# Performance work log

Hardware: AMD Instinct MI355X
Metric: run time of the kernel (lower is better)

Reference implementation:

```python
import jax, jax.numpy as jnp
import numpy as np

N = 1_000_000
C = 128
B = 16  # number of instances (batch segments)
EPS = 1e-5


def setup_inputs() -> dict:
    key = jax.random.key(0)
    k1, k2 = jax.random.split(key)
    x = jax.random.normal(k1, (N, C), dtype=jnp.float32)
    batch_idx = jnp.sort(jax.random.randint(k2, (N,), 0, B, dtype=jnp.int32))
    weight = jnp.ones((1, C), dtype=jnp.float32)
    bias = jnp.zeros((1, C), dtype=jnp.float32)
    return {"x": x, "batch_idx": batch_idx, "weight": weight, "bias": bias}


def reference(x, batch_idx, weight, bias):
    # per-instance counts [B, 1]
    cnt = jax.ops.segment_sum(jnp.ones((x.shape[0], 1), x.dtype), batch_idx,
                              num_segments=B)
    cnt = jnp.maximum(cnt, 1.0)
    # segment mean [B, C]
    mean = jax.ops.segment_sum(x, batch_idx, num_segments=B) / cnt
    centered = x - mean[batch_idx]               # broadcast-add of -mean
    # segment mean of squared centered features -> per-instance variance [B, C]
    var = jax.ops.segment_sum(centered * centered, batch_idx, num_segments=B) / cnt
    instd = 1.0 / jnp.sqrt(var + EPS)            # [B, C]
    # broadcast-multiply, then affine
    return centered * instd[batch_idx] * weight + bias
```

## Files before the change

kernel.cpp:

```cpp
#include <hip/hip_runtime.h>

#define CC 128
#define BSEG 16
#define EPSV 1e-5f
#define ROWS_PER_BLOCK 512
#define NORM_GRID 2048

typedef float v4f __attribute__((ext_vector_type(4)));

__global__ __launch_bounds__(256) void ms_stats(const float* __restrict__ x,
                                                const int* __restrict__ bidx,
                                                int n,
                                                float* __restrict__ sum,
                                                float* __restrict__ sumsq,
                                                float* __restrict__ cnt)
{
    const int r0 = blockIdx.x * ROWS_PER_BLOCK;
    if (r0 >= n) return;
    const int rend = min(r0 + ROWS_PER_BLOCK, n);
    const int tq = threadIdx.x & 31;
    const int tr = threadIdx.x >> 5;

    const int seg_first = bidx[r0];
    const int seg_last  = bidx[rend - 1];

    v4f s = {0.f, 0.f, 0.f, 0.f};
    v4f q = {0.f, 0.f, 0.f, 0.f};

    if (seg_first == seg_last) {
        int r = r0 + tr;
        for (; r + 8 < rend; r += 16) {
            const v4f a = *reinterpret_cast<const v4f*>(x + (size_t)r * CC + tq * 4);
            const v4f b = *reinterpret_cast<const v4f*>(x + (size_t)(r + 8) * CC + tq * 4);
            s += a; q += a * a;
            s += b; q += b * b;
        }
        if (r < rend) {
            const v4f a = *reinterpret_cast<const v4f*>(x + (size_t)r * CC + tq * 4);
            s += a; q += a * a;
        }
        __shared__ float red[8][8][32];
        red[tr][0][tq] = s.x; red[tr][1][tq] = s.y; red[tr][2][tq] = s.z; red[tr][3][tq] = s.w;
        red[tr][4][tq] = q.x; red[tr][5][tq] = q.y; red[tr][6][tq] = q.z; red[tr][7][tq] = q.w;
        __syncthreads();
        const int j = threadIdx.x >> 5;
        float acc = 0.f;
        #pragma unroll
        for (int k = 0; k < 8; ++k) acc += red[k][j][tq];
        const int ch = tq * 4 + (j & 3);
        atomicAdd(((j < 4) ? sum : sumsq) + seg_first * CC + ch, acc);
        if (threadIdx.x == 0)
            atomicAdd(cnt + seg_first, (float)(rend - r0));
    } else {
        int cur = -1;
        float rows = 0.f;
        for (int r = r0 + tr; r < rend; r += 8) {
            const int seg = bidx[r];
            if (seg != cur) {
                if (cur >= 0) {
                    float* sd = sum   + cur * CC + tq * 4;
                    float* qd = sumsq + cur * CC + tq * 4;
                    atomicAdd(sd + 0, s.x); atomicAdd(sd + 1, s.y);
                    atomicAdd(sd + 2, s.z); atomicAdd(sd + 3, s.w);
                    atomicAdd(qd + 0, q.x); atomicAdd(qd + 1, q.y);
                    atomicAdd(qd + 2, q.z); atomicAdd(qd + 3, q.w);
                    if (tq == 0) atomicAdd(cnt + cur, rows);
                    s = (v4f){0.f, 0.f, 0.f, 0.f};
                    q = (v4f){0.f, 0.f, 0.f, 0.f};
                    rows = 0.f;
                }
                cur = seg;
            }
            const v4f a = *reinterpret_cast<const v4f*>(x + (size_t)r * CC + tq * 4);
            s += a; q += a * a;
            rows += 1.f;
        }
        if (cur >= 0) {
            float* sd = sum   + cur * CC + tq * 4;
            float* qd = sumsq + cur * CC + tq * 4;
            atomicAdd(sd + 0, s.x); atomicAdd(sd + 1, s.y);
            atomicAdd(sd + 2, s.z); atomicAdd(sd + 3, s.w);
            atomicAdd(qd + 0, q.x); atomicAdd(qd + 1, q.y);
            atomicAdd(qd + 2, q.z); atomicAdd(qd + 3, q.w);
            if (tq == 0) atomicAdd(cnt + cur, rows);
        }
    }
}

__global__ __launch_bounds__(256) void ms_norm(const float* __restrict__ x,
                                               const int* __restrict__ bidx,
                                               const float* __restrict__ sum,
                                               const float* __restrict__ sumsq,
                                               const float* __restrict__ cnt,
                                               const float* __restrict__ w,
                                               const float* __restrict__ bias,
                                               float* __restrict__ out,
                                               int n)
{
    __shared__ v4f s_scale[BSEG * 32];
    __shared__ v4f s_shift[BSEG * 32];
    for (int i = threadIdx.x; i < BSEG * CC; i += 256) {
        const int b = i >> 7;
        const int c = i & (CC - 1);
        const float nn   = fmaxf(cnt[b], 1.0f);
        const float mean = sum[i] / nn;
        const float var  = fmaxf(sumsq[i] / nn - mean * mean, 0.0f);
        const float sc   = rsqrtf(var + EPSV) * w[c];
        reinterpret_cast<float*>(s_scale)[i] = sc;
        reinterpret_cast<float*>(s_shift)[i] = fmaf(-mean, sc, bias[c]);
    }
    __syncthreads();

    const int total = n * 16;
    const int T     = (int)(gridDim.x * blockDim.x);

    int p = total - 1 - (int)(blockIdx.x * blockDim.x + threadIdx.x);

    for (; p >= 3 * T; p -= 4 * T) {
        const int p0 = p, p1 = p - T, p2 = p - 2 * T, p3 = p - 3 * T;
        const int g0 = bidx[p0 >> 4];
        const int g1 = bidx[p1 >> 4];
        const int g2 = bidx[p2 >> 4];
        const int g3 = bidx[p3 >> 4];
        const v4f a0 = reinterpret_cast<const v4f*>(x)[2 * (size_t)p0];
        const v4f b0 = reinterpret_cast<const v4f*>(x)[2 * (size_t)p0 + 1];
        const v4f a1 = reinterpret_cast<const v4f*>(x)[2 * (size_t)p1];
        const v4f b1 = reinterpret_cast<const v4f*>(x)[2 * (size_t)p1 + 1];
        const v4f a2 = reinterpret_cast<const v4f*>(x)[2 * (size_t)p2];
        const v4f b2 = reinterpret_cast<const v4f*>(x)[2 * (size_t)p2 + 1];
        const v4f a3 = reinterpret_cast<const v4f*>(x)[2 * (size_t)p3];
        const v4f b3 = reinterpret_cast<const v4f*>(x)[2 * (size_t)p3 + 1];

        {
            const int q2i = (p0 & 15) * 2;
            const v4f sca = s_scale[g0 * 32 + q2i], scb = s_scale[g0 * 32 + q2i + 1];
            const v4f sha = s_shift[g0 * 32 + q2i], shb = s_shift[g0 * 32 + q2i + 1];
            v4f oa, ob;
            oa.x = fmaf(a0.x, sca.x, sha.x); oa.y = fmaf(a0.y, sca.y, sha.y);
            oa.z = fmaf(a0.z, sca.z, sha.z); oa.w = fmaf(a0.w, sca.w, sha.w);
            ob.x = fmaf(b0.x, scb.x, shb.x); ob.y = fmaf(b0.y, scb.y, shb.y);
            ob.z = fmaf(b0.z, scb.z, shb.z); ob.w = fmaf(b0.w, scb.w, shb.w);
            __builtin_nontemporal_store(oa, reinterpret_cast<v4f*>(out) + 2 * (size_t)p0);
            __builtin_nontemporal_store(ob, reinterpret_cast<v4f*>(out) + 2 * (size_t)p0 + 1);
        }
        {
            const int q2i = (p1 & 15) * 2;
            const v4f sca = s_scale[g1 * 32 + q2i], scb = s_scale[g1 * 32 + q2i + 1];
            const v4f sha = s_shift[g1 * 32 + q2i], shb = s_shift[g1 * 32 + q2i + 1];
            v4f oa, ob;
            oa.x = fmaf(a1.x, sca.x, sha.x); oa.y = fmaf(a1.y, sca.y, sha.y);
            oa.z = fmaf(a1.z, sca.z, sha.z); oa.w = fmaf(a1.w, sca.w, sha.w);
            ob.x = fmaf(b1.x, scb.x, shb.x); ob.y = fmaf(b1.y, scb.y, shb.y);
            ob.z = fmaf(b1.z, scb.z, shb.z); ob.w = fmaf(b1.w, scb.w, shb.w);
            __builtin_nontemporal_store(oa, reinterpret_cast<v4f*>(out) + 2 * (size_t)p1);
            __builtin_nontemporal_store(ob, reinterpret_cast<v4f*>(out) + 2 * (size_t)p1 + 1);
        }
        {
            const int q2i = (p2 & 15) * 2;
            const v4f sca = s_scale[g2 * 32 + q2i], scb = s_scale[g2 * 32 + q2i + 1];
            const v4f sha = s_shift[g2 * 32 + q2i], shb = s_shift[g2 * 32 + q2i + 1];
            v4f oa, ob;
            oa.x = fmaf(a2.x, sca.x, sha.x); oa.y = fmaf(a2.y, sca.y, sha.y);
            oa.z = fmaf(a2.z, sca.z, sha.z); oa.w = fmaf(a2.w, sca.w, sha.w);
            ob.x = fmaf(b2.x, scb.x, shb.x); ob.y = fmaf(b2.y, scb.y, shb.y);
            ob.z = fmaf(b2.z, scb.z, shb.z); ob.w = fmaf(b2.w, scb.w, shb.w);
            __builtin_nontemporal_store(oa, reinterpret_cast<v4f*>(out) + 2 * (size_t)p2);
            __builtin_nontemporal_store(ob, reinterpret_cast<v4f*>(out) + 2 * (size_t)p2 + 1);
        }
        {
            const int q2i = (p3 & 15) * 2;
            const v4f sca = s_scale[g3 * 32 + q2i], scb = s_scale[g3 * 32 + q2i + 1];
            const v4f sha = s_shift[g3 * 32 + q2i], shb = s_shift[g3 * 32 + q2i + 1];
            v4f oa, ob;
            oa.x = fmaf(a3.x, sca.x, sha.x); oa.y = fmaf(a3.y, sca.y, sha.y);
            oa.z = fmaf(a3.z, sca.z, sha.z); oa.w = fmaf(a3.w, sca.w, sha.w);
            ob.x = fmaf(b3.x, scb.x, shb.x); ob.y = fmaf(b3.y, scb.y, shb.y);
            ob.z = fmaf(b3.z, scb.z, shb.z); ob.w = fmaf(b3.w, scb.w, shb.w);
            __builtin_nontemporal_store(oa, reinterpret_cast<v4f*>(out) + 2 * (size_t)p3);
            __builtin_nontemporal_store(ob, reinterpret_cast<v4f*>(out) + 2 * (size_t)p3 + 1);
        }
    }

    for (; p >= 0; p -= T) {
        const int g = bidx[p >> 4];
        const v4f a = reinterpret_cast<const v4f*>(x)[2 * (size_t)p];
        const v4f b = reinterpret_cast<const v4f*>(x)[2 * (size_t)p + 1];
        const int q2i = (p & 15) * 2;
        const v4f sca = s_scale[g * 32 + q2i], scb = s_scale[g * 32 + q2i + 1];
        const v4f sha = s_shift[g * 32 + q2i], shb = s_shift[g * 32 + q2i + 1];
        v4f oa, ob;
        oa.x = fmaf(a.x, sca.x, sha.x); oa.y = fmaf(a.y, sca.y, sha.y);
        oa.z = fmaf(a.z, sca.z, sha.z); oa.w = fmaf(a.w, sca.w, sha.w);
        ob.x = fmaf(b.x, scb.x, shb.x); ob.y = fmaf(b.y, scb.y, shb.y);
        ob.z = fmaf(b.z, scb.z, shb.z); ob.w = fmaf(b.w, scb.w, shb.w);
        __builtin_nontemporal_store(oa, reinterpret_cast<v4f*>(out) + 2 * (size_t)p);
        __builtin_nontemporal_store(ob, reinterpret_cast<v4f*>(out) + 2 * (size_t)p + 1);
    }
}

extern "C" void kernel_launch(void* const* d_in, const int* in_sizes, int n_in,
                              void* d_out, int out_size, void* d_ws, size_t ws_size,
                              hipStream_t stream)
{
    const float* x    = (const float*)d_in[0];
    const int*   bidx = (const int*)d_in[1];
    const float* w    = (const float*)d_in[2];
    const float* bias = (const float*)d_in[3];
    float* out = (float*)d_out;
    const int n = in_sizes[1];

    float* ws    = (float*)d_ws;
    float* sum   = ws;
    float* sumsq = ws + BSEG * CC;
    float* cnt   = ws + 2 * BSEG * CC;

    (void)hipMemsetAsync(d_ws, 0, (size_t)(2 * BSEG * CC + BSEG) * sizeof(float), stream);

    const int g1 = (n + ROWS_PER_BLOCK - 1) / ROWS_PER_BLOCK;
    ms_stats<<<g1, 256, 0, stream>>>(x, bidx, n, sum, sumsq, cnt);
    ms_norm<<<NORM_GRID, 256, 0, stream>>>(x, bidx, sum, sumsq, cnt, w, bias, out, n);
}
```

Measured before the change: 354.0 us.

## Derive segment counts and boundaries by binary search instead of atomics and gathers

Drops the count atomics from the stats kernel. The norm kernel instead finds the segment boundaries by binary search over the sorted batch index and takes counts from the boundary differences. In the norm loop each element finds its segment by comparing its row against register-held boundaries, replacing the per-element batch-index gather. The loop also loses its 4x manual unroll, which may reduce memory-level parallelism. The change relies on batch_idx being sorted, which the input setup guarantees.

```diff
diff --git a/kernel.cpp b/kernel.cpp
--- a/kernel.cpp
+++ b/kernel.cpp
@@ -8,12 +8,21 @@
 
 typedef float v4f __attribute__((ext_vector_type(4)));
 
+__device__ __forceinline__ int lower_bound_dev(const int* __restrict__ a, int n, int v)
+{
+    int lo = 0, hi = n;
+    while (lo < hi) {
+        const int mid = (lo + hi) >> 1;
+        if (a[mid] < v) lo = mid + 1; else hi = mid;
+    }
+    return lo;
+}
+
 __global__ __launch_bounds__(256) void ms_stats(const float* __restrict__ x,
                                                 const int* __restrict__ bidx,
                                                 int n,
                                                 float* __restrict__ sum,
-                                                float* __restrict__ sumsq,
-                                                float* __restrict__ cnt)
+                                                float* __restrict__ sumsq)
 {
     const int r0 = blockIdx.x * ROWS_PER_BLOCK;
     if (r0 >= n) return;
@@ -49,11 +58,8 @@
         for (int k = 0; k < 8; ++k) acc += red[k][j][tq];
         const int ch = tq * 4 + (j & 3);
         atomicAdd(((j < 4) ? sum : sumsq) + seg_first * CC + ch, acc);
-        if (threadIdx.x == 0)
-            atomicAdd(cnt + seg_first, (float)(rend - r0));
     } else {
         int cur = -1;
-        float rows = 0.f;
         for (int r = r0 + tr; r < rend; r += 8) {
             const int seg = bidx[r];
             if (seg != cur) {
@@ -64,16 +70,13 @@
                     atomicAdd(sd + 2, s.z); atomicAdd(sd + 3, s.w);
                     atomicAdd(qd + 0, q.x); atomicAdd(qd + 1, q.y);
                     atomicAdd(qd + 2, q.z); atomicAdd(qd + 3, q.w);
-                    if (tq == 0) atomicAdd(cnt + cur, rows);
                     s = (v4f){0.f, 0.f, 0.f, 0.f};
                     q = (v4f){0.f, 0.f, 0.f, 0.f};
-                    rows = 0.f;
                 }
                 cur = seg;
             }
             const v4f a = *reinterpret_cast<const v4f*>(x + (size_t)r * CC + tq * 4);
             s += a; q += a * a;
-            rows += 1.f;
         }
         if (cur >= 0) {
             float* sd = sum   + cur * CC + tq * 4;
@@ -82,7 +85,6 @@
             atomicAdd(sd + 2, s.z); atomicAdd(sd + 3, s.w);
             atomicAdd(qd + 0, q.x); atomicAdd(qd + 1, q.y);
             atomicAdd(qd + 2, q.z); atomicAdd(qd + 3, q.w);
-            if (tq == 0) atomicAdd(cnt + cur, rows);
         }
     }
 }
@@ -91,18 +93,23 @@
                                                const int* __restrict__ bidx,
                                                const float* __restrict__ sum,
                                                const float* __restrict__ sumsq,
-                                               const float* __restrict__ cnt,
                                                const float* __restrict__ w,
                                                const float* __restrict__ bias,
                                                float* __restrict__ out,
                                                int n)
 {
+    __shared__ int sbs[BSEG + 1];
     __shared__ v4f s_scale[BSEG * 32];
     __shared__ v4f s_shift[BSEG * 32];
+
+    if (threadIdx.x <= BSEG)
+        sbs[threadIdx.x] = lower_bound_dev(bidx, n, (int)threadIdx.x);
+    __syncthreads();
+
     for (int i = threadIdx.x; i < BSEG * CC; i += 256) {
         const int b = i >> 7;
         const int c = i & (CC - 1);
-        const float nn   = fmaxf(cnt[b], 1.0f);
+        const float nn   = fmaxf((float)(sbs[b + 1] - sbs[b]), 1.0f);
         const float mean = sum[i] / nn;
         const float var  = fmaxf(sumsq[i] / nn - mean * mean, 0.0f);
         const float sc   = rsqrtf(var + EPSV) * w[c];
@@ -111,83 +118,25 @@
     }
     __syncthreads();
 
+    int rb[BSEG - 1];
+    #pragma unroll
+    for (int i = 0; i < BSEG - 1; ++i) rb[i] = sbs[i + 1];
+
     const int total = n * 16;
     const int T     = (int)(gridDim.x * blockDim.x);
 
-    int p = total - 1 - (int)(blockIdx.x * blockDim.x + threadIdx.x);
+    for (int p = total - 1 - (int)(blockIdx.x * blockDim.x + threadIdx.x);
+         p >= 0; p -= T) {
+        const int r = p >> 4;
+        int seg = 0;
+        #pragma unroll
+        for (int i = 0; i < BSEG - 1; ++i) seg += (r >= rb[i]);
 
-    for (; p >= 3 * T; p -= 4 * T) {
-        const int p0 = p, p1 = p - T, p2 = p - 2 * T, p3 = p - 3 * T;
-        const int g0 = bidx[p0 >> 4];
-        const int g1 = bidx[p1 >> 4];
-        const int g2 = bidx[p2 >> 4];
-        const int g3 = bidx[p3 >> 4];
-        const v4f a0 = reinterpret_cast<const v4f*>(x)[2 * (size_t)p0];
-        const v4f b0 = reinterpret_cast<const v4f*>(x)[2 * (size_t)p0 + 1];
-        const v4f a1 = reinterpret_cast<const v4f*>(x)[2 * (size_t)p1];
-        const v4f b1 = reinterpret_cast<const v4f*>(x)[2 * (size_t)p1 + 1];
-        const v4f a2 = reinterpret_cast<const v4f*>(x)[2 * (size_t)p2];
-        const v4f b2 = reinterpret_cast<const v4f*>(x)[2 * (size_t)p2 + 1];
-        const v4f a3 = reinterpret_cast<const v4f*>(x)[2 * (size_t)p3];
-        const v4f b3 = reinterpret_cast<const v4f*>(x)[2 * (size_t)p3 + 1];
-
-        {
-            const int q2i = (p0 & 15) * 2;
-            const v4f sca = s_scale[g0 * 32 + q2i], scb = s_scale[g0 * 32 + q2i + 1];
-            const v4f sha = s_shift[g0 * 32 + q2i], shb = s_shift[g0 * 32 + q2i + 1];
-            v4f oa, ob;
-            oa.x = fmaf(a0.x, sca.x, sha.x); oa.y = fmaf(a0.y, sca.y, sha.y);
-            oa.z = fmaf(a0.z, sca.z, sha.z); oa.w = fmaf(a0.w, sca.w, sha.w);
-            ob.x = fmaf(b0.x, scb.x, shb.x); ob.y = fmaf(b0.y, scb.y, shb.y);
-            ob.z = fmaf(b0.z, scb.z, shb.z); ob.w = fmaf(b0.w, scb.w, shb.w);
-            __builtin_nontemporal_store(oa, reinterpret_cast<v4f*>(out) + 2 * (size_t)p0);
-            __builtin_nontemporal_store(ob, reinterpret_cast<v4f*>(out) + 2 * (size_t)p0 + 1);
-        }
-        {
-            const int q2i = (p1 & 15) * 2;
-            const v4f sca = s_scale[g1 * 32 + q2i], scb = s_scale[g1 * 32 + q2i + 1];
-            const v4f sha = s_shift[g1 * 32 + q2i], shb = s_shift[g1 * 32 + q2i + 1];
-            v4f oa, ob;
-            oa.x = fmaf(a1.x, sca.x, sha.x); oa.y = fmaf(a1.y, sca.y, sha.y);
-            oa.z = fmaf(a1.z, sca.z, sha.z); oa.w = fmaf(a1.w, sca.w, sha.w);
-            ob.x = fmaf(b1.x, scb.x, shb.x); ob.y = fmaf(b1.y, scb.y, shb.y);
-            ob.z = fmaf(b1.z, scb.z, shb.z); ob.w = fmaf(b1.w, scb.w, shb.w);
-            __builtin_nontemporal_store(oa, reinterpret_cast<v4f*>(out) + 2 * (size_t)p1);
-            __builtin_nontemporal_store(ob, reinterpret_cast<v4f*>(out) + 2 * (size_t)p1 + 1);
-        }
-        {
-            const int q2i = (p2 & 15) * 2;
-            const v4f sca = s_scale[g2 * 32 + q2i], scb = s_scale[g2 * 32 + q2i + 1];
-            const v4f sha = s_shift[g2 * 32 + q2i], shb = s_shift[g2 * 32 + q2i + 1];
-            v4f oa, ob;
-            oa.x = fmaf(a2.x, sca.x, sha.x); oa.y = fmaf(a2.y, sca.y, sha.y);
-            oa.z = fmaf(a2.z, sca.z, sha.z); oa.w = fmaf(a2.w, sca.w, sha.w);
-            ob.x = fmaf(b2.x, scb.x, shb.x); ob.y = fmaf(b2.y, scb.y, shb.y);
-            ob.z = fmaf(b2.z, scb.z, shb.z); ob.w = fmaf(b2.w, scb.w, shb.w);
-            __builtin_nontemporal_store(oa, reinterpret_cast<v4f*>(out) + 2 * (size_t)p2);
-            __builtin_nontemporal_store(ob, reinterpret_cast<v4f*>(out) + 2 * (size_t)p2 + 1);
-        }
-        {
-            const int q2i = (p3 & 15) * 2;
-            const v4f sca = s_scale[g3 * 32 + q2i], scb = s_scale[g3 * 32 + q2i + 1];
-            const v4f sha = s_shift[g3 * 32 + q2i], shb = s_shift[g3 * 32 + q2i + 1];
-            v4f oa, ob;
-            oa.x = fmaf(a3.x, sca.x, sha.x); oa.y = fmaf(a3.y, sca.y, sha.y);
-            oa.z = fmaf(a3.z, sca.z, sha.z); oa.w = fmaf(a3.w, sca.w, sha.w);
-            ob.x = fmaf(b3.x, scb.x, shb.x); ob.y = fmaf(b3.y, scb.y, shb.y);
-            ob.z = fmaf(b3.z, scb.z, shb.z); ob.w = fmaf(b3.w, scb.w, shb.w);
-            __builtin_nontemporal_store(oa, reinterpret_cast<v4f*>(out) + 2 * (size_t)p3);
-            __builtin_nontemporal_store(ob, reinterpret_cast<v4f*>(out) + 2 * (size_t)p3 + 1);
-        }
-    }
-
-    for (; p >= 0; p -= T) {
-        const int g = bidx[p >> 4];
         const v4f a = reinterpret_cast<const v4f*>(x)[2 * (size_t)p];
         const v4f b = reinterpret_cast<const v4f*>(x)[2 * (size_t)p + 1];
-        const int q2i = (p & 15) * 2;
-        const v4f sca = s_scale[g * 32 + q2i], scb = s_scale[g * 32 + q2i + 1];
-        const v4f sha = s_shift[g * 32 + q2i], shb = s_shift[g * 32 + q2i + 1];
+        const int ti = seg * 32 + (p & 15) * 2;
+        const v4f sca = s_scale[ti], scb = s_scale[ti + 1];
+        const v4f sha = s_shift[ti], shb = s_shift[ti + 1];
         v4f oa, ob;
         oa.x = fmaf(a.x, sca.x, sha.x); oa.y = fmaf(a.y, sca.y, sha.y);
         oa.z = fmaf(a.z, sca.z, sha.z); oa.w = fmaf(a.w, sca.w, sha.w);
@@ -212,11 +161,10 @@
     float* ws    = (float*)d_ws;
     float* sum   = ws;
     float* sumsq = ws + BSEG * CC;
-    float* cnt   = ws + 2 * BSEG * CC;
 
-    (void)hipMemsetAsync(d_ws, 0, (size_t)(2 * BSEG * CC + BSEG) * sizeof(float), stream);
+    (void)hipMemsetAsync(d_ws, 0, (size_t)(2 * BSEG * CC) * sizeof(float), stream);
 
     const int g1 = (n + ROWS_PER_BLOCK - 1) / ROWS_PER_BLOCK;
-    ms_stats<<<g1, 256, 0, stream>>>(x, bidx, n, sum, sumsq, cnt);
-    ms_norm<<<NORM_GRID, 256, 0, stream>>>(x, bidx, sum, sumsq, cnt, w, bias, out, n);
+    ms_stats<<<g1, 256, 0, stream>>>(x, bidx, n, sum, sumsq);
+    ms_norm<<<NORM_GRID, 256, 0, stream>>>(x, bidx, sum, sumsq, w, bias, out, n);
 }
```

After: 322.4 us. -8.9%, faster.
